# Kernel tuning notes

Measured on AMD Instinct MI355X. Metric: run time of the kernel, lower is better.

Reference implementation:

```python
import jax, jax.numpy as jnp
import numpy as np

D_STATE = 16
D_CONV = 4
DT_RANK = 2  # ceil(d_model/16) with d_model=32


def _conv2d(x, w, b, pad, dil=1, groups=1):
    y = jax.lax.conv_general_dilated(
        x, w, (1, 1), ((pad, pad), (pad, pad)), rhs_dilation=(dil, dil),
        feature_group_count=groups, dimension_numbers=('NCHW', 'OIHW', 'NCHW'))
    return y + b[None, :, None, None]


def _ssm(xc, delta, A, Bc, Cc, D):
    # xc,delta: (B,L,Di); A: (Di,N); Bc,Cc: (B,L,N)
    dA = jnp.exp(delta[..., None] * A)                       # (B,L,Di,N)
    dBx = delta[..., None] * Bc[:, :, None, :] * xc[..., None]
    def comb(e1, e2):
        a1, b1 = e1
        a2, b2 = e2
        return a2 * a1, a2 * b1 + b2
    _, h = jax.lax.associative_scan(comb, (dA, dBx), axis=1)  # h_t = dA_t*h_{t-1}+dBx_t
    return jnp.einsum('bldn,bln->bld', h, Cc) + xc * D


def _dir(xin, cw, cb, wx, wdt, bdt, A_log, D):
    # causal depthwise conv1d over L, then silu
    L = xin.shape[1]
    xp = jnp.pad(xin, ((0, 0), (D_CONV - 1, 0), (0, 0)))
    xc = sum(xp[:, k:k + L, :] * cw[:, k] for k in range(D_CONV)) + cb
    xc = jax.nn.silu(xc)
    dbc = xc @ wx.T                                          # (B,L,dt_rank+2N)
    dt, Bc, Cc = jnp.split(dbc, [DT_RANK, DT_RANK + D_STATE], axis=-1)
    delta = jax.nn.softplus(dt @ wdt.T + bdt)
    return _ssm(xc, delta, -jnp.exp(A_log), Bc, Cc, D)


def _mamba(xn, w_in, cwf, cbf, wxf, wdtf, bdtf, Af, Df,
           cwb, cbb, wxb, wdtb, bdtb, Ab, Db, w_out):
    xz = xn @ w_in.T                                         # (B,L,2*Di)
    xin, z = jnp.split(xz, 2, axis=-1)
    y_f = _dir(xin, cwf, cbf, wxf, wdtf, bdtf, Af, Df)
    y_b = jnp.flip(_dir(jnp.flip(xin, axis=1), cwb, cbb, wxb, wdtb, bdtb, Ab, Db), axis=1)
    return ((y_f + y_b) * jax.nn.silu(z)) @ w_out.T          # bimamba v2: sum of directions


def _forward(x, w_att, b_att, ln_w, ln_b, w_in,
             conv_w_f, conv_b_f, wx_f, wdt_f, bdt_f, A_log_f, D_f,
             conv_w_b, conv_b_b, wx_b, wdt_b, bdt_b, A_log_b, D_b,
             w_out, w_se, b_se, w_conv, b_conv):
    B, C, H, W = x.shape
    att1 = x
    xa = _conv2d(x, w_att, b_att, pad=9, dil=3, groups=C)    # dilated depthwise, same HxW
    xf = xa.reshape(B, C, H * W).transpose(0, 2, 1)          # (B,L,C)
    mu = xf.mean(-1, keepdims=True)
    var = xf.var(-1, keepdims=True)
    xn = (xf - mu) / jnp.sqrt(var + 1e-5) * ln_w + ln_b
    out = _mamba(xn, w_in, conv_w_f, conv_b_f, wx_f, wdt_f, bdt_f, A_log_f, D_f,
                 conv_w_b, conv_b_b, wx_b, wdt_b, bdt_b, A_log_b, D_b, w_out)
    att2 = out.transpose(0, 2, 1).reshape(B, C, H, W)
    att = jnp.concatenate([att1, att2], axis=1)
    pooled = jnp.concatenate([att.mean(1, keepdims=True), att.max(1, keepdims=True)], axis=1)
    se = jax.nn.sigmoid(_conv2d(pooled, w_se, b_se, pad=3))
    output = att1 * se[:, 0:1] + att2 * se[:, 1:2]
    return _conv2d(output, w_conv, b_conv, pad=1)


def setup_inputs() -> dict:
    key = jax.random.key(0)
    ks = jax.random.split(key, 16)
    B, C, H, W = 4, 32, 96, 96
    Di, OUT = 64, 64
    n = jax.random.normal
    A_log = jnp.tile(jnp.log(jnp.arange(1, D_STATE + 1, dtype=jnp.float32)), (Di, 1))
    return {
        'x': n(ks[0], (B, C, H, W), jnp.float32),
        'w_att': n(ks[1], (C, 1, 7, 7), jnp.float32) * 0.05,
        'b_att': jnp.zeros((C,), jnp.float32),
        'ln_w': jnp.ones((C,), jnp.float32),
        'ln_b': jnp.zeros((C,), jnp.float32),
        'w_in': n(ks[2], (2 * Di, C), jnp.float32) / np.sqrt(C),
        'conv_w_f': n(ks[3], (Di, D_CONV), jnp.float32) * 0.3,
        'conv_b_f': jnp.zeros((Di,), jnp.float32),
        'wx_f': n(ks[4], (DT_RANK + 2 * D_STATE, Di), jnp.float32) / np.sqrt(Di),
        'wdt_f': n(ks[5], (Di, DT_RANK), jnp.float32) * 0.5,
        'bdt_f': n(ks[6], (Di,), jnp.float32) * 0.1,
        'A_log_f': A_log,
        'D_f': jnp.ones((Di,), jnp.float32),
        'conv_w_b': n(ks[7], (Di, D_CONV), jnp.float32) * 0.3,
        'conv_b_b': jnp.zeros((Di,), jnp.float32),
        'wx_b': n(ks[8], (DT_RANK + 2 * D_STATE, Di), jnp.float32) / np.sqrt(Di),
        'wdt_b': n(ks[9], (Di, DT_RANK), jnp.float32) * 0.5,
        'bdt_b': n(ks[10], (Di,), jnp.float32) * 0.1,
        'A_log_b': A_log,
        'D_b': jnp.ones((Di,), jnp.float32),
        'w_out': n(ks[11], (C, Di), jnp.float32) / np.sqrt(Di),
        'w_se': n(ks[12], (2, 2, 7, 7), jnp.float32) * 0.1,
        'b_se': jnp.zeros((2,), jnp.float32),
        'w_conv': n(ks[13], (OUT, C, 3, 3), jnp.float32) * 0.06,
        'b_conv': jnp.zeros((OUT,), jnp.float32),
    }


def reference(x, w_att, b_att, ln_w, ln_b, w_in,
              conv_w_f, conv_b_f, wx_f, wdt_f, bdt_f, A_log_f, D_f,
              conv_w_b, conv_b_b, wx_b, wdt_b, bdt_b, A_log_b, D_b,
              w_out, w_se, b_se, w_conv, b_conv):
    return _forward(x, w_att, b_att, ln_w, ln_b, w_in,
                    conv_w_f, conv_b_f, wx_f, wdt_f, bdt_f, A_log_f, D_f,
                    conv_w_b, conv_b_b, wx_b, wdt_b, bdt_b, A_log_b, D_b,
                    w_out, w_se, b_se, w_conv, b_conv)
```

## Files before the change

kernel.cpp:

```cpp
#include <hip/hip_runtime.h>
#include <math.h>

#define BB 4
#define CH 32
#define HH 96
#define WW 96
#define LL (HH*WW)
#define DI 64
#define NS 16
#define BL (BB*LL)
#define NCH 288
#define CLEN (LL/NCH)
#define GG 8

__device__ __forceinline__ float sigmoidf_(float x){ return 1.f/(1.f+__expf(-x)); }
__device__ __forceinline__ float siluf_(float x){ return x*sigmoidf_(x); }
__device__ __forceinline__ float softplusf_(float x){
  return (x > 15.f) ? x : __logf(1.f + __expf(x));
}
#define WAVE_LDS_FENCE() do { asm volatile("s_waitcnt lgkmcnt(0)" ::: "memory"); __builtin_amdgcn_sched_barrier(0); } while(0)

__global__ __launch_bounds__(256) void k1_conv_att(
    const float* __restrict__ x, const float* __restrict__ w,
    const float* __restrict__ bias, float* __restrict__ xa){
  int idx = blockIdx.x*256 + threadIdx.x;
  if (idx >= BB*CH*LL) return;
  int w0 = idx % WW; int h0 = (idx/WW) % HH; int c = (idx/LL) % CH;
  const float* xp = x + (idx/LL)*LL;
  const float* wp = w + c*49;
  float acc = bias[c];
  #pragma unroll
  for (int kh=0; kh<7; ++kh){
    int hh = h0 + 3*kh - 9;
    if ((unsigned)hh >= HH) continue;
    const float* row = xp + hh*WW;
    #pragma unroll
    for (int kw=0; kw<7; ++kw){
      int ww = w0 + 3*kw - 9;
      if ((unsigned)ww < WW) acc += row[ww]*wp[kh*7+kw];
    }
  }
  xa[idx] = acc;
}

__global__ __launch_bounds__(128) void k2_ln_inproj(
    const float* __restrict__ xa, const float* __restrict__ w_in,
    const float* __restrict__ ln_w, const float* __restrict__ ln_b,
    float* __restrict__ xin, float* __restrict__ zs){
  __shared__ float xs[CH*36];
  __shared__ float smu[32], srs[32];
  int tid = threadIdx.x;
  int tg0 = blockIdx.x*32;
  int bb = tg0 / LL;
  int l0 = tg0 % LL;
  const float* xab = xa + bb*CH*LL + l0;
  for (int r=0; r<8; ++r){
    int idx = r*128 + tid;
    int c = idx >> 5, t = idx & 31;
    xs[c*36+t] = xab[c*LL + t];
  }
  int j = tid;
  float wlj[CH];
  float swl=0.f, bj=0.f;
  #pragma unroll
  for (int c=0;c<CH;++c){
    float wv = ln_w[c]*w_in[j*CH+c];
    wlj[c] = wv; swl += wv;
    bj += ln_b[c]*w_in[j*CH+c];
  }
  __syncthreads();
  if (tid < 32){
    float s=0.f, s2=0.f;
    #pragma unroll
    for (int c=0;c<CH;++c){ float v = xs[c*36+tid]; s+=v; s2+=v*v; }
    float mu = s*(1.f/CH);
    float var = s2*(1.f/CH) - mu*mu;
    smu[tid]=mu; srs[tid]=rsqrtf(var+1e-5f);
  }
  __syncthreads();
  for (int t4=0;t4<8;++t4){
    float a0=0.f,a1=0.f,a2=0.f,a3=0.f;
    #pragma unroll
    for (int c=0;c<CH;++c){
      float4 xv = *(const float4*)&xs[c*36 + t4*4];
      float wv = wlj[c];
      a0 += xv.x*wv; a1 += xv.y*wv; a2 += xv.z*wv; a3 += xv.w*wv;
    }
    float av[4] = {a0,a1,a2,a3};
    #pragma unroll
    for (int q=0;q<4;++q){
      int t = t4*4+q;
      float out = srs[t]*(av[q] - smu[t]*swl) + bj;
      int base = ((bb*LL) + l0 + t)*DI;
      if (j < DI) xin[base + j] = out;
      else        zs[base + (j-DI)] = siluf_(out);
    }
  }
}

__global__ __launch_bounds__(64) void k3_fused(
    const float* __restrict__ xin,
    const float* __restrict__ cw_f, const float* __restrict__ cb_f,
    const float* __restrict__ wx_f, const float* __restrict__ wdt_f, const float* __restrict__ bdt_f,
    const float* __restrict__ Al_f,
    const float* __restrict__ cw_b, const float* __restrict__ cb_b,
    const float* __restrict__ wx_b, const float* __restrict__ wdt_b, const float* __restrict__ bdt_b,
    const float* __restrict__ Al_b,
    float* __restrict__ xc_f, float* __restrict__ dl_f, float* __restrict__ Bc_f, float* __restrict__ Cc_f,
    float* __restrict__ xc_b, float* __restrict__ dl_b, float* __restrict__ Bc_b, float* __restrict__ Cc_b,
    float* __restrict__ aggP, float* __restrict__ aggS){
  int lane = threadIdx.x;
  int dir = blockIdx.y;
  int bb = blockIdx.z;
  int ch = blockIdx.x;
  int p0 = ch*CLEN;
  const float* cw  = dir? cw_b : cw_f;
  const float* cb  = dir? cb_b : cb_f;
  const float* wx  = dir? wx_b : wx_f;
  const float* wdt = dir? wdt_b : wdt_f;
  const float* bdt = dir? bdt_b : bdt_f;
  const float* Al  = dir? Al_b : Al_f;
  float* xcbuf = dir? xc_b : xc_f;
  float* dlbuf = dir? dl_b : dl_f;
  float* Bcb   = dir? Bc_b : Bc_f;
  float* Ccb   = dir? Cc_b : Cc_f;

  __shared__ float xcs[GG*64];
  __shared__ float bcs[GG*16];
  __shared__ float dtb[GG*2];

  int d = lane;
  float c0=cw[d*4+0], c1=cw[d*4+1], c2=cw[d*4+2], c3=cw[d*4+3], cbv=cb[d];
  float wd0=wdt[d*2], wd1=wdt[d*2+1], bd=bdt[d];
  float A[NS];
  #pragma unroll
  for (int n4=0;n4<4;++n4){
    float4 av = *(const float4*)&Al[d*NS + n4*4];
    A[n4*4+0] = -__expf(av.x); A[n4*4+1] = -__expf(av.y);
    A[n4*4+2] = -__expf(av.z); A[n4*4+3] = -__expf(av.w);
  }
  float wreg[64];
  if (lane < 34){
    #pragma unroll
    for (int c4=0;c4<16;++c4){
      float4 wv = *(const float4*)&wx[lane*64 + c4*4];
      wreg[c4*4+0]=wv.x; wreg[c4*4+1]=wv.y; wreg[c4*4+2]=wv.z; wreg[c4*4+3]=wv.w;
    }
  }
  float S[NS];
  #pragma unroll
  for (int n=0;n<NS;++n) S[n]=0.f;
  float sdl = 0.f;
  float u1=0.f,u2=0.f,u3=0.f;
  #pragma unroll
  for (int k=1;k<=3;++k){
    int pos = p0 - k;
    float v = 0.f;
    if (pos >= 0){ int ls = dir? (LL-1-pos) : pos; v = xin[(bb*LL+ls)*DI + d]; }
    if(k==1) u1=v; else if(k==2) u2=v; else u3=v;
  }

  for (int g=0; g<CLEN/GG; ++g){
    int pbase = p0 + g*GG;
    float xcr[GG];
    #pragma unroll
    for (int j=0;j<GG;++j){
      int pos = pbase + j;
      int ls = dir? (LL-1-pos) : pos;
      float u0 = xin[(bb*LL+ls)*DI + d];
      float xc = siluf_(cbv + c0*u3 + c1*u2 + c2*u1 + c3*u0);
      u3=u2; u2=u1; u1=u0;
      xcr[j] = xc;
      xcs[j*64+d] = xc;
    }
    #pragma unroll
    for (int j=0;j<GG;++j) xcbuf[(bb*LL+pbase+j)*DI + d] = xcr[j];
    WAVE_LDS_FENCE();
    if (lane < 34){
      #pragma unroll
      for (int j=0;j<GG;++j){
        float acc = 0.f;
        #pragma unroll
        for (int c4=0;c4<16;++c4){
          float4 xv = *(const float4*)&xcs[j*64 + c4*4];
          acc += xv.x*wreg[c4*4+0] + xv.y*wreg[c4*4+1]
               + xv.z*wreg[c4*4+2] + xv.w*wreg[c4*4+3];
        }
        int tb = bb*LL + pbase + j;
        if (lane < 2){
          dtb[j*2+lane] = acc;
        } else if (lane < 18){
          Bcb[tb*NS + lane-2] = acc;
          bcs[j*16 + lane-2] = acc;
        } else {
          Ccb[tb*NS + lane-18] = acc;
        }
      }
    }
    WAVE_LDS_FENCE();
    #pragma unroll
    for (int j=0;j<GG;++j){
      int tb = bb*LL + pbase + j;
      float dlt = softplusf_(dtb[j*2]*wd0 + dtb[j*2+1]*wd1 + bd);
      dlbuf[tb*DI + d] = dlt;
      sdl += dlt;
      float dx = dlt*xcr[j];
      #pragma unroll
      for (int n4=0;n4<4;++n4){
        float4 bv = *(const float4*)&bcs[j*16 + n4*4];
        float bvv[4] = {bv.x,bv.y,bv.z,bv.w};
        #pragma unroll
        for (int q=0;q<4;++q){
          int n = n4*4+q;
          float dA = __expf(dlt*A[n]);
          S[n] = dA*S[n] + dx*bvv[q];
        }
      }
    }
  }
  int bdd = (bb*2+dir)*DI + d;
  float* pp = aggP + (bdd*NCH + ch)*NS;
  float* sp = aggS + (bdd*NCH + ch)*NS;
  #pragma unroll
  for (int n4=0;n4<4;++n4){
    *(float4*)&pp[n4*4] = make_float4(__expf(A[n4*4+0]*sdl),__expf(A[n4*4+1]*sdl),
                                      __expf(A[n4*4+2]*sdl),__expf(A[n4*4+3]*sdl));
    *(float4*)&sp[n4*4] = make_float4(S[n4*4+0],S[n4*4+1],S[n4*4+2],S[n4*4+3]);
  }
}

__global__ __launch_bounds__(256) void p2_scan_agg(
    const float* __restrict__ aggP, const float* __restrict__ aggS,
    float* __restrict__ hin){
  int t = blockIdx.x*256 + threadIdx.x;
  if (t >= BB*2*DI*NS) return;
  int bdd = t >> 4, n = t & 15;
  float h = 0.f;
  #pragma unroll 4
  for (int k=0;k<NCH;++k){
    int i = (bdd*NCH + k)*NS + n;
    float pv = aggP[i], sv = aggS[i];
    hin[i] = h;
    h = pv*h + sv;
  }
}

__global__ __launch_bounds__(64) void p3_scan_out(
    const float* __restrict__ dl_f, const float* __restrict__ xc_f,
    const float* __restrict__ Bc_f, const float* __restrict__ Cc_f,
    const float* __restrict__ dl_b, const float* __restrict__ xc_b,
    const float* __restrict__ Bc_b, const float* __restrict__ Cc_b,
    const float* __restrict__ Al_f, const float* __restrict__ D_f,
    const float* __restrict__ Al_b, const float* __restrict__ D_b,
    const float* __restrict__ hin, float* __restrict__ y_f, float* __restrict__ y_b){
  int lane = threadIdx.x;
  int dir = blockIdx.y >> 1;
  int dhalf = blockIdx.y & 1;
  int bb = blockIdx.z; int ch = blockIdx.x;
  int d = dhalf*32 + (lane & 31);
  int nb = (lane >> 5) * 8;
  const float* dl = dir? dl_b : dl_f;
  const float* xc = dir? xc_b : xc_f;
  const float* Bc = dir? Bc_b : Bc_f;
  const float* Cc = dir? Cc_b : Cc_f;
  const float* Al = dir? Al_b : Al_f;
  const float* Dv = dir? D_b : D_f;
  float* y = dir? y_b : y_f;
  float A[8];
  #pragma unroll
  for (int n4=0;n4<2;++n4){
    float4 av = *(const float4*)&Al[d*NS + nb + n4*4];
    A[n4*4+0] = -__expf(av.x); A[n4*4+1] = -__expf(av.y);
    A[n4*4+2] = -__expf(av.z); A[n4*4+3] = -__expf(av.w);
  }
  float Dd = Dv[d];
  int bdd = (bb*2+dir)*DI + d;
  const float* hp = hin + (bdd*NCH + ch)*NS + nb;
  float h[8];
  #pragma unroll
  for (int n4=0;n4<2;++n4){
    float4 hv = *(const float4*)&hp[n4*4];
    h[n4*4+0]=hv.x; h[n4*4+1]=hv.y; h[n4*4+2]=hv.z; h[n4*4+3]=hv.w;
  }
  int p0 = ch*CLEN;
  #pragma unroll 2
  for (int t=0;t<CLEN;++t){
    int tb = bb*LL + p0 + t;
    float dlt = dl[tb*DI+d];
    float xcv = xc[tb*DI+d];
    float dx = dlt*xcv;
    float4 bv0 = *(const float4*)&Bc[tb*NS + nb];
    float4 bv1 = *(const float4*)&Bc[tb*NS + nb + 4];
    float4 cv0 = *(const float4*)&Cc[tb*NS + nb];
    float4 cv1 = *(const float4*)&Cc[tb*NS + nb + 4];
    float bvv[8]={bv0.x,bv0.y,bv0.z,bv0.w,bv1.x,bv1.y,bv1.z,bv1.w};
    float cvv[8]={cv0.x,cv0.y,cv0.z,cv0.w,cv1.x,cv1.y,cv1.z,cv1.w};
    float pacc[4]={0.f,0.f,0.f,0.f};
    #pragma unroll
    for (int n=0;n<8;++n){
      float dA = __expf(dlt*A[n]);
      h[n] = dA*h[n] + dx*bvv[n];
      pacc[n&3] += h[n]*cvv[n];
    }
    float acc = (pacc[0]+pacc[1]) + (pacc[2]+pacc[3]);
    float other = __shfl_xor(acc, 32, 64);
    if (lane < 32) y[tb*DI + d] = xcv*Dd + acc + other;
  }
}

__global__ __launch_bounds__(256) void k4_outproj(
    const float* __restrict__ y_f, const float* __restrict__ y_b, const float* __restrict__ zs,
    const float* __restrict__ w_out, float* __restrict__ att2){
  __shared__ float gt[32*64];
  __shared__ float wol[32*65];
  __shared__ float ot[32*33];
  int tid = threadIdx.x;
  int tg0 = blockIdx.x*32;
  int bb = tg0/LL, l0 = tg0%LL;
  for (int r=0;r<8;++r){
    int idx = r*256+tid;
    wol[(idx>>6)*65 + (idx&63)] = w_out[idx];
  }
  for (int r=0;r<8;++r){
    int idx = r*256+tid;
    int tk = idx>>6, d = idx&63;
    int l = l0+tk;
    int tbf = (bb*LL + l)*DI + d;
    int tbb = (bb*LL + (LL-1-l))*DI + d;
    gt[idx] = (y_f[tbf] + y_b[tbb]) * zs[tbf];
  }
  __syncthreads();
  int c = tid & 31, tsl = tid >> 5;
  for (int tg=0; tg<4; ++tg){
    int tk = tg*8+tsl;
    float acc=0.f;
    #pragma unroll
    for (int d=0;d<DI;++d) acc += gt[tk*64+d]*wol[c*65+d];
    ot[c*33+tk] = acc;
  }
  __syncthreads();
  float* a2 = att2 + bb*CH*LL + l0;
  for (int r=0;r<4;++r){
    int idx = r*256+tid;
    int cc2 = idx>>5, t = idx&31;
    a2[cc2*LL + t] = ot[cc2*33+t];
  }
}

__global__ __launch_bounds__(256) void k5a_pool(
    const float* __restrict__ x, const float* __restrict__ att2, float* __restrict__ pooled){
  __shared__ float ps[4][64], pm[4][64];
  int tid = threadIdx.x;
  int lq = tid & 63, q = tid >> 6;
  int gl = blockIdx.x*64 + lq;
  int bb = gl/LL, l = gl%LL;
  const float* xp = x + bb*CH*LL + l;
  const float* ap = att2 + bb*CH*LL + l;
  float s=0.f, m=-INFINITY;
  #pragma unroll
  for (int cc=0;cc<8;++cc){
    int c = q*8+cc;
    float v1 = xp[c*LL], v2 = ap[c*LL];
    s += v1+v2;
    m = fmaxf(m, fmaxf(v1,v2));
  }
  ps[q][lq] = s; pm[q][lq] = m;
  __syncthreads();
  if (tid < 64){
    int gl2 = blockIdx.x*64 + tid;
    int bb2 = gl2/LL, l2 = gl2%LL;
    float ss = (ps[0][tid]+ps[1][tid]) + (ps[2][tid]+ps[3][tid]);
    float mm = fmaxf(fmaxf(pm[0][tid],pm[1][tid]), fmaxf(pm[2][tid],pm[3][tid]));
    pooled[(bb2*2+0)*LL + l2] = ss*(1.f/64.f);
    pooled[(bb2*2+1)*LL + l2] = mm;
  }
}

__global__ __launch_bounds__(256) void k5b_se_combine(
    const float* __restrict__ x, const float* __restrict__ att2,
    const float* __restrict__ pooled, const float* __restrict__ w_se,
    const float* __restrict__ b_se, float* __restrict__ outbuf){
  __shared__ float pb[4][64];
  __shared__ float sep[2][64];
  int tid = threadIdx.x;
  int lq = tid & 63, q = tid >> 6;
  int i = q & 1, o = q >> 1;
  int gl = blockIdx.x*64 + lq;
  int bb = gl/LL, l = gl%LL;
  int h0 = l/WW, w0 = l%WW;
  const float* pp = pooled + (bb*2+i)*LL;
  const float* wp = w_se + (o*2+i)*49;
  float a = 0.f;
  #pragma unroll
  for (int kh=0;kh<7;++kh){
    int hh = h0+kh-3; if((unsigned)hh>=HH) continue;
    const float* row = pp + hh*WW;
    #pragma unroll
    for (int kw=0;kw<7;++kw){
      int ww2 = w0+kw-3;
      if((unsigned)ww2<WW) a += row[ww2]*wp[kh*7+kw];
    }
  }
  pb[q][lq] = a;
  __syncthreads();
  if (tid < 128){
    int oo = tid >> 6, l2 = tid & 63;
    sep[oo][l2] = sigmoidf_(b_se[oo] + pb[oo*2+0][l2] + pb[oo*2+1][l2]);
  }
  __syncthreads();
  float se0 = sep[0][lq], se1 = sep[1][lq];
  const float* xp = x + bb*CH*LL + l;
  const float* ap = att2 + bb*CH*LL + l;
  float* op = outbuf + bb*CH*LL + l;
  #pragma unroll
  for (int cc=0;cc<8;++cc){
    int c = q*8+cc;
    op[c*LL] = xp[c*LL]*se0 + ap[c*LL]*se1;
  }
}

__global__ __launch_bounds__(256) void k6_conv3x3(
    const float* __restrict__ inb, const float* __restrict__ wc,
    const float* __restrict__ bc, float* __restrict__ out){
  __shared__ float lds[CH*3*98];
  int tid = threadIdx.x;
  int h = blockIdx.x, cohalf = blockIdx.y, bb = blockIdx.z;
  const float* ib = inb + bb*CH*LL;
  for (int r=0; r<36; ++r){
    int idx = r*256+tid;
    int ci = idx/(3*96); int rr = (idx/96)%3; int ww2 = idx%96;
    int hh = h + rr - 1;
    float v = ((unsigned)hh < HH) ? ib[ci*LL + hh*WW + ww2] : 0.f;
    lds[(ci*3+rr)*98 + 1 + ww2] = v;
  }
  if (tid < 96){
    int ci = tid/3, rr = tid%3;
    lds[(ci*3+rr)*98 + 0]  = 0.f;
    lds[(ci*3+rr)*98 + 97] = 0.f;
  }
  __syncthreads();
  int coslot = tid >> 4, wslot = tid & 15;
  int co0 = cohalf*32 + coslot*2, wb = wslot*6;
  float acc[2][6];
  #pragma unroll
  for (int q=0;q<2;++q)
    #pragma unroll
    for (int j2=0;j2<6;++j2) acc[q][j2]=0.f;
  for (int ci=0; ci<CH; ++ci){
    float wt[2][9];
    #pragma unroll
    for (int q=0;q<2;++q){
      const float* wp = wc + ((co0+q)*CH + ci)*9;
      #pragma unroll
      for (int k=0;k<9;++k) wt[q][k] = wp[k];
    }
    #pragma unroll
    for (int kh=0;kh<3;++kh){
      const float* row = &lds[(ci*3+kh)*98 + wb];
      float s[8];
      #pragma unroll
      for (int t2=0;t2<8;++t2) s[t2] = row[t2];
      #pragma unroll
      for (int q=0;q<2;++q)
        #pragma unroll
        for (int kw=0;kw<3;++kw){
          float wv = wt[q][kh*3+kw];
          #pragma unroll
          for (int j2=0;j2<6;++j2) acc[q][j2] += s[j2+kw]*wv;
        }
    }
  }
  #pragma unroll
  for (int q=0;q<2;++q){
    int co = co0+q;
    float bv = bc[co];
    float* op = out + (bb*64 + co)*LL + h*WW + wb;
    #pragma unroll
    for (int j2=0;j2<6;++j2) op[j2] = acc[q][j2]+bv;
  }
}

extern "C" void kernel_launch(void* const* d_in, const int* in_sizes, int n_in,
                              void* d_out, int out_size, void* d_ws, size_t ws_size,
                              hipStream_t stream){
  const float* x     = (const float*)d_in[0];
  const float* w_att = (const float*)d_in[1];
  const float* b_att = (const float*)d_in[2];
  const float* ln_w  = (const float*)d_in[3];
  const float* ln_b  = (const float*)d_in[4];
  const float* w_in  = (const float*)d_in[5];
  const float* cw_f  = (const float*)d_in[6];
  const float* cb_f  = (const float*)d_in[7];
  const float* wx_f  = (const float*)d_in[8];
  const float* wdt_f = (const float*)d_in[9];
  const float* bdt_f = (const float*)d_in[10];
  const float* Al_f  = (const float*)d_in[11];
  const float* D_f   = (const float*)d_in[12];
  const float* cw_b  = (const float*)d_in[13];
  const float* cb_b  = (const float*)d_in[14];
  const float* wx_b  = (const float*)d_in[15];
  const float* wdt_b = (const float*)d_in[16];
  const float* bdt_b = (const float*)d_in[17];
  const float* Al_b  = (const float*)d_in[18];
  const float* D_b   = (const float*)d_in[19];
  const float* w_out = (const float*)d_in[20];
  const float* w_se  = (const float*)d_in[21];
  const float* b_se  = (const float*)d_in[22];
  const float* w_conv= (const float*)d_in[23];
  const float* b_conv= (const float*)d_in[24];

  float* ws = (float*)d_ws;
  float* xa     = ws + 0;
  float* att2   = ws + 0;
  float* xin    = ws + 1179648;
  float* hin    = ws + 1179648;
  float* outbuf = ws + 1179648;
  float* pooled = ws + 3538944;
  float* zs     = ws + 3612672;
  float* xc_f   = ws + 5971968;
  float* xc_b   = ws + 8331264;
  float* dl_f   = ws + 10690560;
  float* dl_b   = ws + 13049856;
  float* Bc_f   = ws + 15409152;
  float* Bc_b   = ws + 15998976;
  float* Cc_f   = ws + 16588800;
  float* Cc_b   = ws + 17178624;
  float* y_f    = ws + 17768448;
  float* y_b    = ws + 20127744;
  float* aggP   = y_f;
  float* aggS   = y_b;

  k1_conv_att<<<4608,256,0,stream>>>(x, w_att, b_att, xa);
  k2_ln_inproj<<<1152,128,0,stream>>>(xa, w_in, ln_w, ln_b, xin, zs);
  k3_fused<<<dim3(NCH,2,BB),64,0,stream>>>(xin,
      cw_f,cb_f,wx_f,wdt_f,bdt_f,Al_f, cw_b,cb_b,wx_b,wdt_b,bdt_b,Al_b,
      xc_f,dl_f,Bc_f,Cc_f, xc_b,dl_b,Bc_b,Cc_b, aggP,aggS);
  p2_scan_agg<<<32,256,0,stream>>>(aggP,aggS,hin);
  p3_scan_out<<<dim3(NCH,4,BB),64,0,stream>>>(dl_f,xc_f,Bc_f,Cc_f, dl_b,xc_b,Bc_b,Cc_b,
      Al_f,D_f, Al_b,D_b, hin, y_f,y_b);
  k4_outproj<<<1152,256,0,stream>>>(y_f,y_b,zs,w_out,att2);
  k5a_pool<<<576,256,0,stream>>>(x, att2, pooled);
  k5b_se_combine<<<576,256,0,stream>>>(x, att2, pooled, w_se, b_se, outbuf);
  k6_conv3x3<<<dim3(HH,2,BB),256,0,stream>>>(outbuf, w_conv, b_conv, (float*)d_out);
}
```

Measured before the change: 325.0 us.

## Compute local SSM outputs in chunk pass and apply carry-in correction in outproj

```diff
diff --git a/kernel.cpp b/kernel.cpp
--- a/kernel.cpp
+++ b/kernel.cpp
@@ -102,12 +102,12 @@
     const float* __restrict__ xin,
     const float* __restrict__ cw_f, const float* __restrict__ cb_f,
     const float* __restrict__ wx_f, const float* __restrict__ wdt_f, const float* __restrict__ bdt_f,
-    const float* __restrict__ Al_f,
+    const float* __restrict__ Al_f, const float* __restrict__ D_f,
     const float* __restrict__ cw_b, const float* __restrict__ cb_b,
     const float* __restrict__ wx_b, const float* __restrict__ wdt_b, const float* __restrict__ bdt_b,
-    const float* __restrict__ Al_b,
-    float* __restrict__ xc_f, float* __restrict__ dl_f, float* __restrict__ Bc_f, float* __restrict__ Cc_f,
-    float* __restrict__ xc_b, float* __restrict__ dl_b, float* __restrict__ Bc_b, float* __restrict__ Cc_b,
+    const float* __restrict__ Al_b, const float* __restrict__ D_b,
+    float* __restrict__ yl_f, float* __restrict__ sp_f, float* __restrict__ Cc_f,
+    float* __restrict__ yl_b, float* __restrict__ sp_b, float* __restrict__ Cc_b,
     float* __restrict__ aggP, float* __restrict__ aggS){
   int lane = threadIdx.x;
   int dir = blockIdx.y;
@@ -120,18 +120,20 @@
   const float* wdt = dir? wdt_b : wdt_f;
   const float* bdt = dir? bdt_b : bdt_f;
   const float* Al  = dir? Al_b : Al_f;
-  float* xcbuf = dir? xc_b : xc_f;
-  float* dlbuf = dir? dl_b : dl_f;
-  float* Bcb   = dir? Bc_b : Bc_f;
+  const float* Dv  = dir? D_b : D_f;
+  float* ylbuf = dir? yl_b : yl_f;
+  float* spbuf = dir? sp_b : sp_f;
   float* Ccb   = dir? Cc_b : Cc_f;
 
   __shared__ float xcs[GG*64];
   __shared__ float bcs[GG*16];
+  __shared__ float ccs[GG*16];
   __shared__ float dtb[GG*2];
 
   int d = lane;
   float c0=cw[d*4+0], c1=cw[d*4+1], c2=cw[d*4+2], c3=cw[d*4+3], cbv=cb[d];
   float wd0=wdt[d*2], wd1=wdt[d*2+1], bd=bdt[d];
+  float Dd = Dv[d];
   float A[NS];
   #pragma unroll
   for (int n4=0;n4<4;++n4){
@@ -160,21 +162,34 @@
     if(k==1) u1=v; else if(k==2) u2=v; else u3=v;
   }
 
-  for (int g=0; g<CLEN/GG; ++g){
+  const int NG = CLEN/GG;
+  float u0buf[GG], u0nxt[GG];
+  #pragma unroll
+  for (int j=0;j<GG;++j){
+    int pos = p0 + j;
+    int ls = dir? (LL-1-pos) : pos;
+    u0buf[j] = xin[(bb*LL+ls)*DI + d];
+  }
+  #pragma unroll
+  for (int g=0; g<NG; ++g){
     int pbase = p0 + g*GG;
+    if (g+1 < NG){
+      #pragma unroll
+      for (int j=0;j<GG;++j){
+        int pos = pbase + GG + j;
+        int ls = dir? (LL-1-pos) : pos;
+        u0nxt[j] = xin[(bb*LL+ls)*DI + d];
+      }
+    }
     float xcr[GG];
     #pragma unroll
     for (int j=0;j<GG;++j){
-      int pos = pbase + j;
-      int ls = dir? (LL-1-pos) : pos;
-      float u0 = xin[(bb*LL+ls)*DI + d];
+      float u0 = u0buf[j];
       float xc = siluf_(cbv + c0*u3 + c1*u2 + c2*u1 + c3*u0);
       u3=u2; u2=u1; u1=u0;
       xcr[j] = xc;
       xcs[j*64+d] = xc;
     }
-    #pragma unroll
-    for (int j=0;j<GG;++j) xcbuf[(bb*LL+pbase+j)*DI + d] = xcr[j];
     WAVE_LDS_FENCE();
     if (lane < 34){
       #pragma unroll
@@ -190,10 +205,10 @@
         if (lane < 2){
           dtb[j*2+lane] = acc;
         } else if (lane < 18){
-          Bcb[tb*NS + lane-2] = acc;
           bcs[j*16 + lane-2] = acc;
         } else {
           Ccb[tb*NS + lane-18] = acc;
+          ccs[j*16 + lane-18] = acc;
         }
       }
     }
@@ -202,21 +217,28 @@
     for (int j=0;j<GG;++j){
       int tb = bb*LL + pbase + j;
       float dlt = softplusf_(dtb[j*2]*wd0 + dtb[j*2+1]*wd1 + bd);
-      dlbuf[tb*DI + d] = dlt;
       sdl += dlt;
+      spbuf[tb*DI + d] = sdl;
       float dx = dlt*xcr[j];
+      float yv = xcr[j]*Dd;
       #pragma unroll
       for (int n4=0;n4<4;++n4){
         float4 bv = *(const float4*)&bcs[j*16 + n4*4];
+        float4 cv = *(const float4*)&ccs[j*16 + n4*4];
         float bvv[4] = {bv.x,bv.y,bv.z,bv.w};
+        float cvv[4] = {cv.x,cv.y,cv.z,cv.w};
         #pragma unroll
         for (int q=0;q<4;++q){
           int n = n4*4+q;
           float dA = __expf(dlt*A[n]);
           S[n] = dA*S[n] + dx*bvv[q];
+          yv += S[n]*cvv[q];
         }
       }
-    }
+      ylbuf[tb*DI + d] = yv;
+    }
+    #pragma unroll
+    for (int j=0;j<GG;++j) u0buf[j] = u0nxt[j];
   }
   int bdd = (bb*2+dir)*DI + d;
   float* pp = aggP + (bdd*NCH + ch)*NS;
@@ -245,89 +267,70 @@
   }
 }
 
-__global__ __launch_bounds__(64) void p3_scan_out(
-    const float* __restrict__ dl_f, const float* __restrict__ xc_f,
-    const float* __restrict__ Bc_f, const float* __restrict__ Cc_f,
-    const float* __restrict__ dl_b, const float* __restrict__ xc_b,
-    const float* __restrict__ Bc_b, const float* __restrict__ Cc_b,
-    const float* __restrict__ Al_f, const float* __restrict__ D_f,
-    const float* __restrict__ Al_b, const float* __restrict__ D_b,
-    const float* __restrict__ hin, float* __restrict__ y_f, float* __restrict__ y_b){
-  int lane = threadIdx.x;
-  int dir = blockIdx.y >> 1;
-  int dhalf = blockIdx.y & 1;
-  int bb = blockIdx.z; int ch = blockIdx.x;
-  int d = dhalf*32 + (lane & 31);
-  int nb = (lane >> 5) * 8;
-  const float* dl = dir? dl_b : dl_f;
-  const float* xc = dir? xc_b : xc_f;
-  const float* Bc = dir? Bc_b : Bc_f;
-  const float* Cc = dir? Cc_b : Cc_f;
-  const float* Al = dir? Al_b : Al_f;
-  const float* Dv = dir? D_b : D_f;
-  float* y = dir? y_b : y_f;
-  float A[8];
-  #pragma unroll
-  for (int n4=0;n4<2;++n4){
-    float4 av = *(const float4*)&Al[d*NS + nb + n4*4];
-    A[n4*4+0] = -__expf(av.x); A[n4*4+1] = -__expf(av.y);
-    A[n4*4+2] = -__expf(av.z); A[n4*4+3] = -__expf(av.w);
-  }
-  float Dd = Dv[d];
-  int bdd = (bb*2+dir)*DI + d;
-  const float* hp = hin + (bdd*NCH + ch)*NS + nb;
-  float h[8];
-  #pragma unroll
-  for (int n4=0;n4<2;++n4){
-    float4 hv = *(const float4*)&hp[n4*4];
-    h[n4*4+0]=hv.x; h[n4*4+1]=hv.y; h[n4*4+2]=hv.z; h[n4*4+3]=hv.w;
-  }
-  int p0 = ch*CLEN;
-  #pragma unroll 2
-  for (int t=0;t<CLEN;++t){
-    int tb = bb*LL + p0 + t;
-    float dlt = dl[tb*DI+d];
-    float xcv = xc[tb*DI+d];
-    float dx = dlt*xcv;
-    float4 bv0 = *(const float4*)&Bc[tb*NS + nb];
-    float4 bv1 = *(const float4*)&Bc[tb*NS + nb + 4];
-    float4 cv0 = *(const float4*)&Cc[tb*NS + nb];
-    float4 cv1 = *(const float4*)&Cc[tb*NS + nb + 4];
-    float bvv[8]={bv0.x,bv0.y,bv0.z,bv0.w,bv1.x,bv1.y,bv1.z,bv1.w};
-    float cvv[8]={cv0.x,cv0.y,cv0.z,cv0.w,cv1.x,cv1.y,cv1.z,cv1.w};
-    float pacc[4]={0.f,0.f,0.f,0.f};
-    #pragma unroll
-    for (int n=0;n<8;++n){
-      float dA = __expf(dlt*A[n]);
-      h[n] = dA*h[n] + dx*bvv[n];
-      pacc[n&3] += h[n]*cvv[n];
-    }
-    float acc = (pacc[0]+pacc[1]) + (pacc[2]+pacc[3]);
-    float other = __shfl_xor(acc, 32, 64);
-    if (lane < 32) y[tb*DI + d] = xcv*Dd + acc + other;
-  }
-}
-
 __global__ __launch_bounds__(256) void k4_outproj(
-    const float* __restrict__ y_f, const float* __restrict__ y_b, const float* __restrict__ zs,
+    const float* __restrict__ yl_f, const float* __restrict__ yl_b,
+    const float* __restrict__ sp_f, const float* __restrict__ sp_b,
+    const float* __restrict__ Cc_f, const float* __restrict__ Cc_b,
+    const float* __restrict__ Al_f, const float* __restrict__ Al_b,
+    const float* __restrict__ hin, const float* __restrict__ zs,
     const float* __restrict__ w_out, float* __restrict__ att2){
+  __shared__ float ccs_f[32*16], ccs_b[32*16];
   __shared__ float gt[32*64];
   __shared__ float wol[32*65];
   __shared__ float ot[32*33];
   int tid = threadIdx.x;
   int tg0 = blockIdx.x*32;
   int bb = tg0/LL, l0 = tg0%LL;
+  int d = tid & 63, tslot = tid >> 6;
   for (int r=0;r<8;++r){
     int idx = r*256+tid;
     wol[(idx>>6)*65 + (idx&63)] = w_out[idx];
   }
+  {
+    int base_f = (bb*LL + l0)*NS;
+    int base_b = (bb*LL + (LL-32-l0))*NS;
+    #pragma unroll
+    for (int r=0;r<2;++r){
+      int idx = r*256+tid;
+      ccs_f[idx] = Cc_f[base_f+idx];
+      ccs_b[idx] = Cc_b[base_b+idx];
+    }
+  }
+  int ch_f = l0/CLEN;
+  int ch_b = (LL-32-l0)/CLEN;
+  const float* hpf = hin + (((bb*2+0)*DI + d)*NCH + ch_f)*NS;
+  const float* hpb = hin + (((bb*2+1)*DI + d)*NCH + ch_b)*NS;
+  float Af[NS], Ab[NS], hf[NS], hb[NS];
+  #pragma unroll
+  for (int n4=0;n4<4;++n4){
+    float4 av = *(const float4*)&Al_f[d*NS + n4*4];
+    Af[n4*4+0]=-__expf(av.x); Af[n4*4+1]=-__expf(av.y);
+    Af[n4*4+2]=-__expf(av.z); Af[n4*4+3]=-__expf(av.w);
+    float4 aw = *(const float4*)&Al_b[d*NS + n4*4];
+    Ab[n4*4+0]=-__expf(aw.x); Ab[n4*4+1]=-__expf(aw.y);
+    Ab[n4*4+2]=-__expf(aw.z); Ab[n4*4+3]=-__expf(aw.w);
+    float4 hv = *(const float4*)&hpf[n4*4];
+    hf[n4*4+0]=hv.x; hf[n4*4+1]=hv.y; hf[n4*4+2]=hv.z; hf[n4*4+3]=hv.w;
+    float4 hw = *(const float4*)&hpb[n4*4];
+    hb[n4*4+0]=hw.x; hb[n4*4+1]=hw.y; hb[n4*4+2]=hw.z; hb[n4*4+3]=hw.w;
+  }
+  __syncthreads();
+  #pragma unroll
   for (int r=0;r<8;++r){
-    int idx = r*256+tid;
-    int tk = idx>>6, d = idx&63;
-    int l = l0+tk;
-    int tbf = (bb*LL + l)*DI + d;
-    int tbb = (bb*LL + (LL-1-l))*DI + d;
-    gt[idx] = (y_f[tbf] + y_b[tbb]) * zs[tbf];
+    int tk = tslot*8 + r;
+    int l = l0 + tk;
+    int tf  = (bb*LL + l)*DI + d;
+    int tb2 = (bb*LL + (LL-1-l))*DI + d;
+    float spf = sp_f[tf],  yf = yl_f[tf];
+    float spb = sp_b[tb2], yb = yl_b[tb2];
+    int jb = 31 - tk;
+    float fixf = 0.f, fixb = 0.f;
+    #pragma unroll
+    for (int n=0;n<NS;++n){
+      fixf += ccs_f[tk*16+n] * (hf[n]*__expf(Af[n]*spf));
+      fixb += ccs_b[jb*16+n] * (hb[n]*__expf(Ab[n]*spb));
+    }
+    gt[tk*64+d] = (yf+fixf + yb+fixb) * zs[tf];
   }
   __syncthreads();
   int c = tid & 31, tsl = tid >> 5;
@@ -335,7 +338,7 @@
     int tk = tg*8+tsl;
     float acc=0.f;
     #pragma unroll
-    for (int d=0;d<DI;++d) acc += gt[tk*64+d]*wol[c*65+d];
+    for (int dd=0;dd<DI;++dd) acc += gt[tk*64+dd]*wol[c*65+dd];
     ot[c*33+tk] = acc;
   }
   __syncthreads();
@@ -513,32 +516,28 @@
   float* xa     = ws + 0;
   float* att2   = ws + 0;
   float* xin    = ws + 1179648;
-  float* hin    = ws + 1179648;
   float* outbuf = ws + 1179648;
-  float* pooled = ws + 3538944;
-  float* zs     = ws + 3612672;
-  float* xc_f   = ws + 5971968;
-  float* xc_b   = ws + 8331264;
-  float* dl_f   = ws + 10690560;
-  float* dl_b   = ws + 13049856;
-  float* Bc_f   = ws + 15409152;
-  float* Bc_b   = ws + 15998976;
-  float* Cc_f   = ws + 16588800;
-  float* Cc_b   = ws + 17178624;
-  float* y_f    = ws + 17768448;
-  float* y_b    = ws + 20127744;
-  float* aggP   = y_f;
-  float* aggS   = y_b;
+  float* zs     = ws + 3538944;
+  float* yl_f   = ws + 5898240;
+  float* yl_b   = ws + 8257536;
+  float* sp_f   = ws + 10616832;
+  float* sp_b   = ws + 12976128;
+  float* Cc_f   = ws + 15335424;
+  float* Cc_b   = ws + 15925248;
+  float* aggP   = ws + 16515072;
+  float* aggS   = ws + 18874368;
+  float* hin    = ws + 21233664;
+  float* pooled = ws + 23592960;
 
   k1_conv_att<<<4608,256,0,stream>>>(x, w_att, b_att, xa);
   k2_ln_inproj<<<1152,128,0,stream>>>(xa, w_in, ln_w, ln_b, xin, zs);
   k3_fused<<<dim3(NCH,2,BB),64,0,stream>>>(xin,
-      cw_f,cb_f,wx_f,wdt_f,bdt_f,Al_f, cw_b,cb_b,wx_b,wdt_b,bdt_b,Al_b,
-      xc_f,dl_f,Bc_f,Cc_f, xc_b,dl_b,Bc_b,Cc_b, aggP,aggS);
+      cw_f,cb_f,wx_f,wdt_f,bdt_f,Al_f,D_f,
+      cw_b,cb_b,wx_b,wdt_b,bdt_b,Al_b,D_b,
+      yl_f,sp_f,Cc_f, yl_b,sp_b,Cc_b, aggP,aggS);
   p2_scan_agg<<<32,256,0,stream>>>(aggP,aggS,hin);
-  p3_scan_out<<<dim3(NCH,4,BB),64,0,stream>>>(dl_f,xc_f,Bc_f,Cc_f, dl_b,xc_b,Bc_b,Cc_b,
-      Al_f,D_f, Al_b,D_b, hin, y_f,y_b);
-  k4_outproj<<<1152,256,0,stream>>>(y_f,y_b,zs,w_out,att2);
+  k4_outproj<<<1152,256,0,stream>>>(yl_f,yl_b, sp_f,sp_b, Cc_f,Cc_b,
+      Al_f,Al_b, hin, zs, w_out, att2);
   k5a_pool<<<576,256,0,stream>>>(x, att2, pooled);
   k5b_se_combine<<<576,256,0,stream>>>(x, att2, pooled, w_se, b_se, outbuf);
   k6_conv3x3<<<dim3(HH,2,BB),256,0,stream>>>(outbuf, w_conv, b_conv, (float*)d_out);
```

After: 342.9 us. +5.5%, slower.
